# Kernel optimization log

Measured on AMD Instinct MI355X. Metric: run time of the kernel, lower is better.

The kernel has to match this reference:

```python
import jax, jax.numpy as jnp
import numpy as np

B, T, D, H, FC, A = 256, 128, 512, 1024, 1024, 32
LOG_STD_MIN, LOG_STD_MAX = -20.0, 2.0
EPS = 1e-5


def setup_inputs() -> dict:
    key = jax.random.key(0)
    ks = jax.random.split(key, 16)
    def w(k, shape, fan_in):
        return jax.random.normal(k, shape, jnp.float32) / np.float32(np.sqrt(fan_in))
    return {
        "observations": jax.random.normal(ks[0], (B, T, D), jnp.float32),
        "hidden_state": jax.random.normal(ks[1], (B, H), jnp.float32),
        "episode_starts": jax.random.randint(ks[2], (B, T), 0, 2, jnp.int32),
        "ln_gamma": jnp.ones((D,), jnp.float32),
        "ln_beta": jnp.zeros((D,), jnp.float32),
        "W_fc": w(ks[3], (FC, D), D), "b_fc": jnp.zeros((FC,), jnp.float32),
        "W_ih": w(ks[4], (3 * H, FC), FC), "b_ih": jnp.zeros((3 * H,), jnp.float32),
        "W_hh": w(ks[5], (3 * H, H), H), "b_hh": jnp.zeros((3 * H,), jnp.float32),
        "W_out": w(ks[6], (H, H), H), "b_out": jnp.zeros((H,), jnp.float32),
        "W_mean": w(ks[7], (A, H), H) * 0.01, "b_mean": jnp.zeros((A,), jnp.float32),
        "W_ls": w(ks[8], (A, H), H) * 0.01, "b_ls": jnp.zeros((A,), jnp.float32),
    }


def reference(observations, hidden_state, episode_starts, ln_gamma, ln_beta,
              W_fc, b_fc, W_ih, b_ih, W_hh, b_hh, W_out, b_out,
              W_mean, b_mean, W_ls, b_ls):
    # LayerNorm over last dim (eps=1e-5, like nn.LayerNorm)
    mu = jnp.mean(observations, axis=-1, keepdims=True)
    var = jnp.mean(jnp.square(observations - mu), axis=-1, keepdims=True)
    x = (observations - mu) * jax.lax.rsqrt(var + EPS) * ln_gamma + ln_beta
    # fc_in + ReLU, then precompute GRU input-gate projections for all steps
    x = jax.nn.relu(jnp.einsum('btd,fd->btf', x, W_fc) + b_fc)          # (B,T,FC)
    xg = jnp.einsum('btf,gf->btg', x, W_ih) + b_ih                      # (B,T,3H)
    xg_t = jnp.swapaxes(xg, 0, 1)                                       # (T,B,3H)
    starts_t = jnp.swapaxes(episode_starts, 0, 1).astype(jnp.float32)   # (T,B)

    def step(h, inp):
        xg_s, st = inp
        h = h * (1.0 - st)[:, None]
        gh = h @ W_hh.T + b_hh                                           # (B,3H)
        xr, xz, xn = xg_s[:, :H], xg_s[:, H:2 * H], xg_s[:, 2 * H:]
        hr, hz, hn = gh[:, :H], gh[:, H:2 * H], gh[:, 2 * H:]
        r = jax.nn.sigmoid(xr + hr)
        z = jax.nn.sigmoid(xz + hz)
        n = jnp.tanh(xn + r * hn)
        h_new = (1.0 - z) * n + z * h
        out = jax.nn.relu(h_new @ W_out.T + b_out)
        return h_new, out

    h_final, outs = jax.lax.scan(step, hidden_state, (xg_t, starts_t))
    feats = jnp.swapaxes(outs, 0, 1)                                     # (B,T,H)
    means = jnp.einsum('bth,ah->bta', feats, W_mean) + b_mean
    log_std = jnp.clip(jnp.einsum('bth,ah->bta', feats, W_ls) + b_ls,
                       LOG_STD_MIN, LOG_STD_MAX)
    return means, log_std, h_final
```

## Files before the change

kernel.cpp:

```cpp
#include <hip/hip_runtime.h>
#include <hip/hip_bf16.h>

#define B_ 256
#define T_ 128
#define D_ 512
#define H_ 1024
#define FC_ 1024
#define A_ 32
#define NWG_ 256

typedef short bf16x8 __attribute__((ext_vector_type(8)));
typedef float f32x4 __attribute__((ext_vector_type(4)));

__device__ __forceinline__ float bf2f(unsigned short u) {
  return __uint_as_float(((unsigned)u) << 16);
}
__device__ __forceinline__ unsigned short f2bf(float x) {
  unsigned u = __float_as_uint(x);
  u = u + 0x7fffu + ((u >> 16) & 1u);
  return (unsigned short)(u >> 16);
}
__device__ __forceinline__ void unpack8(uint4 v, float* f) {
  f[0] = bf2f(v.x & 0xffff); f[1] = bf2f(v.x >> 16);
  f[2] = bf2f(v.y & 0xffff); f[3] = bf2f(v.y >> 16);
  f[4] = bf2f(v.z & 0xffff); f[5] = bf2f(v.z >> 16);
  f[6] = bf2f(v.w & 0xffff); f[7] = bf2f(v.w >> 16);
}
__device__ __forceinline__ uint4 pack8(const float* f) {
  uint4 v;
  v.x = (unsigned)f2bf(f[0]) | ((unsigned)f2bf(f[1]) << 16);
  v.y = (unsigned)f2bf(f[2]) | ((unsigned)f2bf(f[3]) << 16);
  v.z = (unsigned)f2bf(f[4]) | ((unsigned)f2bf(f[5]) << 16);
  v.w = (unsigned)f2bf(f[6]) | ((unsigned)f2bf(f[7]) << 16);
  return v;
}

__global__ __launch_bounds__(256) void detect_kernel(
    const unsigned short* __restrict__ obs, int* __restrict__ flag)
{
  __shared__ int cnt;
  if (threadIdx.x == 0) cnt = 0;
  __syncthreads();
  int c = 0;
  for (int i = threadIdx.x; i < 8192; i += 256) {
    unsigned e = (obs[i] >> 7) & 0xffu;
    if (e >= 0x86u) c++;
  }
  atomicAdd(&cnt, c);
  __syncthreads();
  if (threadIdx.x == 0) *flag = (cnt >= 64) ? 1 : 0;
}

struct CanonArgs {
  const void* src[14];
  unsigned short* dst[14];
  int ofs[15];
};
__global__ __launch_bounds__(256) void canon_kernel(CanonArgs a,
                                                    const int* __restrict__ flag)
{
  const int fl = *flag;
  const int i0 = (blockIdx.x * 256 + threadIdx.x) * 8;
  int t = 0;
  while (t < 14 && i0 >= a.ofs[t + 1]) t++;
  if (t >= 14) return;
  const int local = i0 - a.ofs[t];
  unsigned short* d = a.dst[t] + local;
  if (fl) {
    const float* s = (const float*)a.src[t] + local;
    #pragma unroll
    for (int e = 0; e < 8; e++) d[e] = f2bf(s[e]);
  } else {
    const unsigned short* s = (const unsigned short*)a.src[t] + local;
    #pragma unroll
    for (int e = 0; e < 8; e++) d[e] = s[e];
  }
}

__global__ __launch_bounds__(256) void ln_kernel(
    const void* __restrict__ obs,
    const unsigned short* __restrict__ gamma_,
    const unsigned short* __restrict__ beta_,
    unsigned short* __restrict__ xn, int t0, int tcShift,
    const int* __restrict__ flag)
{
  const int fl = *flag;
  const int lane = threadIdx.x & 63;
  const int rloc = blockIdx.x * 4 + (threadIdx.x >> 6);
  const int b  = rloc >> tcShift;
  const int tl = rloc & ((1 << tcShift) - 1);
  const int grow = b * T_ + t0 + tl;
  float f[8];
  if (fl) {
    const float* of = (const float*)obs + (size_t)grow * D_ + lane * 8;
    const float4 v0 = *(const float4*)of;
    const float4 v1 = *(const float4*)(of + 4);
    f[0] = v0.x; f[1] = v0.y; f[2] = v0.z; f[3] = v0.w;
    f[4] = v1.x; f[5] = v1.y; f[6] = v1.z; f[7] = v1.w;
  } else {
    uint4 v = *(const uint4*)((const unsigned short*)obs + (size_t)grow * D_ + lane * 8);
    unpack8(v, f);
  }
  float s = 0.f, ss = 0.f;
  #pragma unroll
  for (int i = 0; i < 8; i++) { s += f[i]; ss += f[i] * f[i]; }
  #pragma unroll
  for (int off = 32; off > 0; off >>= 1) {
    s  += __shfl_xor(s,  off, 64);
    ss += __shfl_xor(ss, off, 64);
  }
  const float mu  = s * (1.0f / D_);
  const float var = ss * (1.0f / D_) - mu * mu;
  const float inv = rsqrtf(var + 1e-5f);
  float g[8], b8[8];
  unpack8(*(const uint4*)(gamma_ + lane * 8), g);
  unpack8(*(const uint4*)(beta_  + lane * 8), b8);
  float o[8];
  #pragma unroll
  for (int i = 0; i < 8; i++) o[i] = (f[i] - mu) * inv * g[i] + b8[i];
  *(uint4*)(xn + (size_t)rloc * D_ + lane * 8) = pack8(o);
}

__global__ __launch_bounds__(256) void gemm_tn(
    const unsigned short* __restrict__ A, const unsigned short* __restrict__ Bm,
    const unsigned short* __restrict__ bias, unsigned short* __restrict__ C,
    int M, int N, int K, int relu)
{
  __shared__ short As[128][40];
  __shared__ short Bs[128][40];
  const int tid  = threadIdx.x;
  const int wave = tid >> 6, lane = tid & 63;
  const int quad = lane >> 4, l15 = lane & 15;
  const int m0 = blockIdx.y * 128, n0 = blockIdx.x * 128;
  const int wm = (wave >> 1) * 64, wn = (wave & 1) * 64;
  const int lrow = tid >> 2, lk = (tid & 3) * 8;
  f32x4 acc[4][4] = {};
  const size_t a0 = (size_t)(m0 + lrow) * K + lk;
  const size_t a1 = (size_t)(m0 + lrow + 64) * K + lk;
  const size_t b0 = (size_t)(n0 + lrow) * K + lk;
  const size_t b1 = (size_t)(n0 + lrow + 64) * K + lk;
  for (int k0 = 0; k0 < K; k0 += 32) {
    __syncthreads();
    *(uint4*)&As[lrow][lk]      = *(const uint4*)(A  + a0 + k0);
    *(uint4*)&As[lrow + 64][lk] = *(const uint4*)(A  + a1 + k0);
    *(uint4*)&Bs[lrow][lk]      = *(const uint4*)(Bm + b0 + k0);
    *(uint4*)&Bs[lrow + 64][lk] = *(const uint4*)(Bm + b1 + k0);
    __syncthreads();
    bf16x8 af[4], bfv[4];
    #pragma unroll
    for (int i = 0; i < 4; i++) af[i]  = *(const bf16x8*)&As[wm + i * 16 + l15][quad * 8];
    #pragma unroll
    for (int j = 0; j < 4; j++) bfv[j] = *(const bf16x8*)&Bs[wn + j * 16 + l15][quad * 8];
    #pragma unroll
    for (int i = 0; i < 4; i++)
      #pragma unroll
      for (int j = 0; j < 4; j++)
        acc[i][j] = __builtin_amdgcn_mfma_f32_16x16x32_bf16(af[i], bfv[j], acc[i][j], 0, 0, 0);
  }
  #pragma unroll
  for (int j = 0; j < 4; j++) {
    const int col = n0 + wn + j * 16 + l15;
    const float bj = bias ? bf2f(bias[col]) : 0.0f;
    #pragma unroll
    for (int i = 0; i < 4; i++) {
      const int row = m0 + wm + i * 16 + quad * 4;
      #pragma unroll
      for (int r = 0; r < 4; r++) {
        float v = acc[i][j][r] + bj;
        if (relu) v = fmaxf(v, 0.0f);
        C[(size_t)(row + r) * N + col] = f2bf(v);
      }
    }
  }
}

__global__ __launch_bounds__(256, 1) void gru_scan(
    const unsigned short* __restrict__ xg,
    const int* __restrict__ starts,
    const unsigned short* __restrict__ Whh,
    const unsigned short* __restrict__ bhh,
    float* __restrict__ hf,
    unsigned long long* __restrict__ hb0,
    unsigned long long* __restrict__ hb1,
    unsigned short* __restrict__ hall,
    int t0, int Tc,
    int* __restrict__ flags)
{
  __shared__ short Ws[3 * 16 * 1032];
  __shared__ short Hs[64 * 136];
  __shared__ unsigned sbits[64][4];
  const int tid  = threadIdx.x;
  const int wg   = blockIdx.x;
  const int jb   = wg & 63, bb = wg >> 6;
  const int j0   = jb * 16, b0 = bb * 64;
  const int wave = tid >> 6, lane = tid & 63;
  const int quad = lane >> 4, l15 = lane & 15;

  for (int c = tid; c < 48 * 128; c += 256) {
    const int row = c >> 7;
    const int kc  = (c & 127) * 8;
    const int g = row >> 4, jj = row & 15;
    *(uint4*)&Ws[row * 1032 + kc] =
        *(const uint4*)(Whh + (size_t)(g * H_ + j0 + jj) * H_ + kc);
  }
  for (int c = tid; c < 64 * 4; c += 256) {
    const int row = c >> 2, w = c & 3;
    unsigned m = 0;
    #pragma unroll
    for (int bi = 0; bi < 32; bi++)
      m |= (starts[(b0 + row) * T_ + w * 32 + bi] ? 1u : 0u) << bi;
    sbits[row][w] = m;
  }
  const float br = bf2f(bhh[j0 + l15]);
  const float bz = bf2f(bhh[H_ + j0 + l15]);
  const float bn = bf2f(bhh[2 * H_ + j0 + l15]);
  const int col = j0 + l15;

  const int r0 = wave * 16 + quad * 4;
  float hreg[4];
  #pragma unroll
  for (int r = 0; r < 4; r++)
    hreg[r] = hf[(size_t)(b0 + r0 + r) * H_ + col];

  __syncthreads();

  for (int tl = 0; tl < Tc; tl++) {
    const int t = t0 + tl;
    const unsigned long long* hin = (t & 1) ? hb1 : hb0;
    unsigned* hout_u = (unsigned*)((t & 1) ? hb0 : hb1);

    float xr[4], xz[4], xnv[4];
    #pragma unroll
    for (int r = 0; r < 4; r++) {
      const size_t xrow = ((size_t)(b0 + r0 + r) * Tc + tl) * (3 * H_);
      xr[r]  = bf2f(xg[xrow + col]);
      xz[r]  = bf2f(xg[xrow + H_ + col]);
      xnv[r] = bf2f(xg[xrow + 2 * H_ + col]);
    }

    unsigned long long pf[8];
    #pragma unroll
    for (int u = 0; u < 8; u++) {
      const int c = tid + u * 256;
      const int row = c >> 5, kc = (c & 31) * 4;
      pf[u] = __hip_atomic_load(
          &hin[(((size_t)(b0 + row)) * H_ + kc) >> 2],
          __ATOMIC_RELAXED, __HIP_MEMORY_SCOPE_AGENT);
    }

    f32x4 acc[3] = {};
    const unsigned tw = (unsigned)(t >> 5), tb = (unsigned)(t & 31);
    for (int kc0 = 0; kc0 < H_; kc0 += 128) {
      __syncthreads();
      #pragma unroll
      for (int u = 0; u < 8; u++) {
        const int c = tid + u * 256;
        const int row = c >> 5, kc = (c & 31) * 4;
        unsigned long long v = pf[u];
        if ((sbits[row][tw] >> tb) & 1u) v = 0ull;
        *(unsigned long long*)&Hs[row * 136 + kc] = v;
      }
      __syncthreads();
      if (kc0 + 128 < H_) {
        #pragma unroll
        for (int u = 0; u < 8; u++) {
          const int c = tid + u * 256;
          const int row = c >> 5, kc = (c & 31) * 4;
          pf[u] = __hip_atomic_load(
              &hin[(((size_t)(b0 + row)) * H_ + kc0 + 128 + kc) >> 2],
              __ATOMIC_RELAXED, __HIP_MEMORY_SCOPE_AGENT);
        }
      }
      #pragma unroll
      for (int kk = 0; kk < 128; kk += 32) {
        bf16x8 a = *(const bf16x8*)&Hs[(wave * 16 + l15) * 136 + kk + quad * 8];
        #pragma unroll
        for (int g = 0; g < 3; g++) {
          bf16x8 b = *(const bf16x8*)&Ws[(g * 16 + l15) * 1032 + kc0 + kk + quad * 8];
          acc[g] = __builtin_amdgcn_mfma_f32_16x16x32_bf16(a, b, acc[g], 0, 0, 0);
        }
      }
    }

    #pragma unroll
    for (int r = 0; r < 4; r++) {
      const int lrow = r0 + r;
      const int b = b0 + lrow;
      const float kb = ((sbits[lrow][tw] >> tb) & 1u) ? 0.0f : 1.0f;
      const float hr = acc[0][r] + br;
      const float hz = acc[1][r] + bz;
      const float hn = acc[2][r] + bn;
      const float rg = 1.0f / (1.0f + __expf(-(xr[r] + hr)));
      const float zg = 1.0f / (1.0f + __expf(-(xz[r] + hz)));
      const float ng = tanhf(xnv[r] + rg * hn);
      const float hv = (1.0f - zg) * ng + zg * (hreg[r] * kb);
      hreg[r] = hv;
      const unsigned mine = (unsigned)f2bf(hv);
      const unsigned other = (unsigned)__shfl_xor((int)mine, 1, 64);
      if ((l15 & 1) == 0) {
        const unsigned packed = mine | (other << 16);
        __hip_atomic_store(&hout_u[((size_t)b * H_ + col) >> 1], packed,
                           __ATOMIC_RELAXED, __HIP_MEMORY_SCOPE_AGENT);
        ((unsigned*)hall)[(((size_t)b * Tc + tl) * H_ + col) >> 1] = packed;
      }
    }

    const int my = t0 + tl + 1;
    __builtin_amdgcn_s_waitcnt(0);
    __syncthreads();
    if (tid == 0)
      __hip_atomic_store(&flags[wg * 32], my, __ATOMIC_RELAXED,
                         __HIP_MEMORY_SCOPE_AGENT);
    if (tid < 64) {
      while (__hip_atomic_load(&flags[(bb * 64 + tid) * 32], __ATOMIC_RELAXED,
                               __HIP_MEMORY_SCOPE_AGENT) < my)
        __builtin_amdgcn_s_sleep(1);
    }
    __syncthreads();
  }

  #pragma unroll
  for (int r = 0; r < 4; r++)
    hf[(size_t)(b0 + r0 + r) * H_ + col] = hreg[r];
}

__global__ __launch_bounds__(256) void heads_kernel(
    const unsigned short* __restrict__ feats,
    const unsigned short* __restrict__ Wm, const unsigned short* __restrict__ bm,
    const unsigned short* __restrict__ Wl, const unsigned short* __restrict__ bl,
    void* __restrict__ outbuf, int t0, int tcShift, const int* __restrict__ flag)
{
  __shared__ short Fs[64][40];
  __shared__ short Ws[64][40];
  const int fl = *flag;
  const int tid  = threadIdx.x;
  const int wave = tid >> 6, lane = tid & 63;
  const int quad = lane >> 4, l15 = lane & 15;
  const int m0 = blockIdx.x * 64;
  const int lrow = tid >> 2, lk = (tid & 3) * 8;
  f32x4 acc[4] = {};
  for (int k0 = 0; k0 < H_; k0 += 32) {
    __syncthreads();
    *(uint4*)&Fs[lrow][lk] = *(const uint4*)(feats + (size_t)(m0 + lrow) * H_ + k0 + lk);
    const unsigned short* wsrc = (lrow < 32)
        ? (Wm + (size_t)lrow * H_ + k0 + lk)
        : (Wl + (size_t)(lrow - 32) * H_ + k0 + lk);
    *(uint4*)&Ws[lrow][lk] = *(const uint4*)wsrc;
    __syncthreads();
    bf16x8 af = *(const bf16x8*)&Fs[wave * 16 + l15][quad * 8];
    #pragma unroll
    for (int j = 0; j < 4; j++) {
      bf16x8 bfv = *(const bf16x8*)&Ws[j * 16 + l15][quad * 8];
      acc[j] = __builtin_amdgcn_mfma_f32_16x16x32_bf16(af, bfv, acc[j], 0, 0, 0);
    }
  }
  const int tcMask = (1 << tcShift) - 1;
  const size_t lstdBase = (size_t)B_ * T_ * A_;
  #pragma unroll
  for (int j = 0; j < 4; j++) {
    const int col = j * 16 + l15;
    #pragma unroll
    for (int r = 0; r < 4; r++) {
      const int row = m0 + wave * 16 + quad * 4 + r;
      const int grow = (row >> tcShift) * T_ + t0 + (row & tcMask);
      float v = acc[j][r];
      size_t idx;
      if (col < 32) {
        v += bf2f(bm[col]);
        idx = (size_t)grow * A_ + col;
      } else {
        v += bf2f(bl[col - 32]);
        v = fminf(fmaxf(v, -20.0f), 2.0f);
        idx = lstdBase + (size_t)grow * A_ + (col - 32);
      }
      if (fl) ((float*)outbuf)[idx] = v;
      else    ((unsigned short*)outbuf)[idx] = f2bf(v);
    }
  }
}

__global__ __launch_bounds__(256) void h0_cast(const void* __restrict__ h0,
                                               float* __restrict__ hf,
                                               unsigned short* __restrict__ hb0,
                                               const int* __restrict__ flag) {
  const int fl = *flag;
  int i = blockIdx.x * 256 + threadIdx.x;
  float v = fl ? ((const float*)h0)[i] : bf2f(((const unsigned short*)h0)[i]);
  hf[i] = v;
  hb0[i] = f2bf(v);
}
__global__ __launch_bounds__(256) void hfin_store(const float* __restrict__ h,
                                                  void* __restrict__ outbuf,
                                                  const int* __restrict__ flag) {
  const int fl = *flag;
  const size_t base = 2ull * B_ * T_ * A_;
  int i = blockIdx.x * 256 + threadIdx.x;
  if (fl) ((float*)outbuf)[base + i] = h[i];
  else    ((unsigned short*)outbuf)[base + i] = f2bf(h[i]);
}

extern "C" void kernel_launch(void* const* d_in, const int* in_sizes, int n_in,
                              void* d_out, int out_size, void* d_ws, size_t ws_size,
                              hipStream_t stream)
{
  const void* obs    = d_in[0];
  const void* h0in   = d_in[1];
  const int*  starts = (const int*)d_in[2];
  const void* fsrc[14] = { d_in[5], d_in[7], d_in[9], d_in[11], d_in[13], d_in[15],
                           d_in[3], d_in[4], d_in[6], d_in[8], d_in[10], d_in[12],
                           d_in[14], d_in[16] };
  const int fn[14] = { FC_ * D_, 3 * H_ * FC_, 3 * H_ * H_, H_ * H_, A_ * H_, A_ * H_,
                       D_, D_, FC_, 3 * H_, 3 * H_, H_, A_, A_ };

  char* ws = (char*)d_ws;
  int* flag = (int*)ws;
  size_t cur = 256;
  unsigned short* cdst[14];
  for (int i = 0; i < 14; i++) {
    cdst[i] = (unsigned short*)(ws + cur);
    cur += (size_t)fn[i] * 2;
    cur = (cur + 255) & ~255ull;
  }
  const size_t chunkBase = cur;
  const size_t fixedTail = 1048576ull  + 2ull * 524288ull
                         + 32768ull ;

  int Tc = 1;
  for (int c = 32; c >= 1; c >>= 1) {
    size_t need = chunkBase + (size_t)c * 2883584ull + fixedTail;
    if (need <= ws_size) { Tc = c; break; }
  }
  int tcShift = 0;
  while ((1 << tcShift) < Tc) tcShift++;

  unsigned short* xn   = (unsigned short*)(ws + chunkBase);
  unsigned short* xfc  = (unsigned short*)(ws + chunkBase + (size_t)Tc * 262144ull);
  unsigned short* xg   = (unsigned short*)(ws + chunkBase + (size_t)Tc * 786432ull);
  unsigned short* hall = (unsigned short*)(ws + chunkBase + (size_t)Tc * 2359296ull);
  size_t o = chunkBase + (size_t)Tc * 2883584ull;
  float* hf           = (float*)(ws + o);           o += 1048576ull;
  unsigned short* hb0 = (unsigned short*)(ws + o);  o += 524288ull;
  unsigned short* hb1 = (unsigned short*)(ws + o);  o += 524288ull;
  int* flags          = (int*)(ws + o);
  unsigned short* feats = xg;

  const unsigned short *Wfc = cdst[0], *Wih = cdst[1], *Whh = cdst[2], *Wout = cdst[3];
  const unsigned short *Wmean = cdst[4], *Wls = cdst[5];
  const unsigned short *gam = cdst[6], *bet = cdst[7], *bfc = cdst[8], *bih = cdst[9];
  const unsigned short *bhh = cdst[10], *bout = cdst[11], *bmean = cdst[12], *bls = cdst[13];

  detect_kernel<<<dim3(1), dim3(256), 0, stream>>>((const unsigned short*)obs, flag);
  CanonArgs ca;
  int total = 0;
  for (int i = 0; i < 14; i++) {
    ca.src[i] = fsrc[i];
    ca.dst[i] = cdst[i];
    ca.ofs[i] = total;
    total += fn[i];
  }
  ca.ofs[14] = total;
  canon_kernel<<<dim3((total / 8 + 255) / 256), dim3(256), 0, stream>>>(ca, flag);
  h0_cast<<<dim3(B_ * H_ / 256), dim3(256), 0, stream>>>(h0in, hf, hb0, flag);
  hipMemsetAsync(flags, 0, 32768, stream);

  const int Mc = B_ * Tc;
  for (int t0 = 0; t0 < T_; t0 += Tc) {
    ln_kernel<<<dim3(Mc / 4), dim3(256), 0, stream>>>(obs, gam, bet, xn, t0, tcShift, flag);
    gemm_tn<<<dim3(FC_ / 128, Mc / 128), dim3(256), 0, stream>>>(
        xn, Wfc, bfc, xfc, Mc, FC_, D_, 1);
    gemm_tn<<<dim3(3 * H_ / 128, Mc / 128), dim3(256), 0, stream>>>(
        xfc, Wih, bih, xg, Mc, 3 * H_, FC_, 0);

    gru_scan<<<dim3(NWG_), dim3(256), 0, stream>>>(
        xg, starts, Whh, bhh, hf,
        (unsigned long long*)hb0, (unsigned long long*)hb1,
        hall, t0, Tc, flags);

    gemm_tn<<<dim3(H_ / 128, Mc / 128), dim3(256), 0, stream>>>(
        hall, Wout, bout, feats, Mc, H_, H_, 1);
    heads_kernel<<<dim3(Mc / 64), dim3(256), 0, stream>>>(
        feats, Wmean, bmean, Wls, bls, d_out, t0, tcShift, flag);
  }

  hfin_store<<<dim3(B_ * H_ / 256), dim3(256), 0, stream>>>(hf, d_out, flag);
}
```

Before: 1.885 ms.

## Load GRU hidden state directly into registers; use global_load_lds in GEMM

The GRU scan no longer stages the hidden state through shared memory with per-chunk barriers. Each wave now loads its own 16 rows of h straight into registers in MFMA operand layout, applies the episode-start mask with a bitwise AND, and runs all 32 k-steps without any syncthreads. Separately, the tiled GEMM uses direct global-to-LDS loads with an unpadded LDS layout, dropping the register round trip. The trade-offs are much higher register pressure in the scan (64 u64 values per lane) and possible LDS bank conflicts now that the GEMM tile rows are no longer padded.

```diff
diff --git a/kernel.cpp b/kernel.cpp
--- a/kernel.cpp
+++ b/kernel.cpp
@@ -11,6 +11,8 @@
 
 typedef short bf16x8 __attribute__((ext_vector_type(8)));
 typedef float f32x4 __attribute__((ext_vector_type(4)));
+typedef unsigned long long ull;
+typedef ull ullx2 __attribute__((ext_vector_type(2)));
 
 __device__ __forceinline__ float bf2f(unsigned short u) {
   return __uint_as_float(((unsigned)u) << 16);
@@ -126,31 +128,42 @@
     const unsigned short* __restrict__ bias, unsigned short* __restrict__ C,
     int M, int N, int K, int relu)
 {
-  __shared__ short As[128][40];
-  __shared__ short Bs[128][40];
+  __shared__ short As[128 * 32];
+  __shared__ short Bs[128 * 32];
   const int tid  = threadIdx.x;
   const int wave = tid >> 6, lane = tid & 63;
   const int quad = lane >> 4, l15 = lane & 15;
   const int m0 = blockIdx.y * 128, n0 = blockIdx.x * 128;
   const int wm = (wave >> 1) * 64, wn = (wave & 1) * 64;
-  const int lrow = tid >> 2, lk = (tid & 3) * 8;
+  const int srow = tid >> 2;
+  const int skc  = (tid & 3) * 8;
+  const size_t aoff0 = (size_t)(m0 + srow) * K + skc;
+  const size_t aoff1 = (size_t)(m0 + 64 + srow) * K + skc;
+  const size_t boff0 = (size_t)(n0 + srow) * K + skc;
+  const size_t boff1 = (size_t)(n0 + 64 + srow) * K + skc;
+  const int lb0 = wave * 512;
+  const int lb1 = 2048 + wave * 512;
   f32x4 acc[4][4] = {};
-  const size_t a0 = (size_t)(m0 + lrow) * K + lk;
-  const size_t a1 = (size_t)(m0 + lrow + 64) * K + lk;
-  const size_t b0 = (size_t)(n0 + lrow) * K + lk;
-  const size_t b1 = (size_t)(n0 + lrow + 64) * K + lk;
   for (int k0 = 0; k0 < K; k0 += 32) {
     __syncthreads();
-    *(uint4*)&As[lrow][lk]      = *(const uint4*)(A  + a0 + k0);
-    *(uint4*)&As[lrow + 64][lk] = *(const uint4*)(A  + a1 + k0);
-    *(uint4*)&Bs[lrow][lk]      = *(const uint4*)(Bm + b0 + k0);
-    *(uint4*)&Bs[lrow + 64][lk] = *(const uint4*)(Bm + b1 + k0);
+    __builtin_amdgcn_global_load_lds(
+        (const __attribute__((address_space(1))) unsigned*)(A + aoff0 + k0),
+        (__attribute__((address_space(3))) unsigned*)&As[lb0], 16, 0, 0);
+    __builtin_amdgcn_global_load_lds(
+        (const __attribute__((address_space(1))) unsigned*)(A + aoff1 + k0),
+        (__attribute__((address_space(3))) unsigned*)&As[lb1], 16, 0, 0);
+    __builtin_amdgcn_global_load_lds(
+        (const __attribute__((address_space(1))) unsigned*)(Bm + boff0 + k0),
+        (__attribute__((address_space(3))) unsigned*)&Bs[lb0], 16, 0, 0);
+    __builtin_amdgcn_global_load_lds(
+        (const __attribute__((address_space(1))) unsigned*)(Bm + boff1 + k0),
+        (__attribute__((address_space(3))) unsigned*)&Bs[lb1], 16, 0, 0);
     __syncthreads();
     bf16x8 af[4], bfv[4];
     #pragma unroll
-    for (int i = 0; i < 4; i++) af[i]  = *(const bf16x8*)&As[wm + i * 16 + l15][quad * 8];
-    #pragma unroll
-    for (int j = 0; j < 4; j++) bfv[j] = *(const bf16x8*)&Bs[wn + j * 16 + l15][quad * 8];
+    for (int i = 0; i < 4; i++) af[i]  = *(const bf16x8*)&As[(wm + i * 16 + l15) * 32 + quad * 8];
+    #pragma unroll
+    for (int j = 0; j < 4; j++) bfv[j] = *(const bf16x8*)&Bs[(wn + j * 16 + l15) * 32 + quad * 8];
     #pragma unroll
     for (int i = 0; i < 4; i++)
       #pragma unroll
@@ -180,14 +193,13 @@
     const unsigned short* __restrict__ Whh,
     const unsigned short* __restrict__ bhh,
     float* __restrict__ hf,
-    unsigned long long* __restrict__ hb0,
-    unsigned long long* __restrict__ hb1,
+    ull* __restrict__ hb0,
+    ull* __restrict__ hb1,
     unsigned short* __restrict__ hall,
     int t0, int Tc,
     int* __restrict__ flags)
 {
   __shared__ short Ws[3 * 16 * 1032];
-  __shared__ short Hs[64 * 136];
   __shared__ unsigned sbits[64][4];
   const int tid  = threadIdx.x;
   const int wg   = blockIdx.x;
@@ -222,12 +234,29 @@
   for (int r = 0; r < 4; r++)
     hreg[r] = hf[(size_t)(b0 + r0 + r) * H_ + col];
 
+  const int arow = wave * 16 + l15;
+  const size_t hrowbase = ((size_t)(b0 + arow)) << 8;
+  const short* wsb = &Ws[l15 * 1032 + quad * 8];
+
   __syncthreads();
 
   for (int tl = 0; tl < Tc; tl++) {
     const int t = t0 + tl;
-    const unsigned long long* hin = (t & 1) ? hb1 : hb0;
+    const ull* hin = (t & 1) ? hb1 : hb0;
     unsigned* hout_u = (unsigned*)((t & 1) ? hb0 : hb1);
+    const unsigned tw = (unsigned)(t >> 5), tb = (unsigned)(t & 31);
+
+    ull hu0[32], hu1[32];
+    {
+      const ull* hp = hin + hrowbase + quad * 2;
+      #pragma unroll
+      for (int j = 0; j < 32; j++) {
+        hu0[j] = __hip_atomic_load(hp + j * 8,     __ATOMIC_RELAXED,
+                                   __HIP_MEMORY_SCOPE_AGENT);
+        hu1[j] = __hip_atomic_load(hp + j * 8 + 1, __ATOMIC_RELAXED,
+                                   __HIP_MEMORY_SCOPE_AGENT);
+      }
+    }
 
     float xr[4], xz[4], xnv[4];
     #pragma unroll
@@ -238,48 +267,21 @@
       xnv[r] = bf2f(xg[xrow + 2 * H_ + col]);
     }
 
-    unsigned long long pf[8];
-    #pragma unroll
-    for (int u = 0; u < 8; u++) {
-      const int c = tid + u * 256;
-      const int row = c >> 5, kc = (c & 31) * 4;
-      pf[u] = __hip_atomic_load(
-          &hin[(((size_t)(b0 + row)) * H_ + kc) >> 2],
-          __ATOMIC_RELAXED, __HIP_MEMORY_SCOPE_AGENT);
-    }
+    const ull keep = ((sbits[arow][tw] >> tb) & 1u) ? 0ull : ~0ull;
 
     f32x4 acc[3] = {};
-    const unsigned tw = (unsigned)(t >> 5), tb = (unsigned)(t & 31);
-    for (int kc0 = 0; kc0 < H_; kc0 += 128) {
-      __syncthreads();
-      #pragma unroll
-      for (int u = 0; u < 8; u++) {
-        const int c = tid + u * 256;
-        const int row = c >> 5, kc = (c & 31) * 4;
-        unsigned long long v = pf[u];
-        if ((sbits[row][tw] >> tb) & 1u) v = 0ull;
-        *(unsigned long long*)&Hs[row * 136 + kc] = v;
-      }
-      __syncthreads();
-      if (kc0 + 128 < H_) {
-        #pragma unroll
-        for (int u = 0; u < 8; u++) {
-          const int c = tid + u * 256;
-          const int row = c >> 5, kc = (c & 31) * 4;
-          pf[u] = __hip_atomic_load(
-              &hin[(((size_t)(b0 + row)) * H_ + kc0 + 128 + kc) >> 2],
-              __ATOMIC_RELAXED, __HIP_MEMORY_SCOPE_AGENT);
-        }
-      }
-      #pragma unroll
-      for (int kk = 0; kk < 128; kk += 32) {
-        bf16x8 a = *(const bf16x8*)&Hs[(wave * 16 + l15) * 136 + kk + quad * 8];
-        #pragma unroll
-        for (int g = 0; g < 3; g++) {
-          bf16x8 b = *(const bf16x8*)&Ws[(g * 16 + l15) * 1032 + kc0 + kk + quad * 8];
-          acc[g] = __builtin_amdgcn_mfma_f32_16x16x32_bf16(a, b, acc[g], 0, 0, 0);
-        }
-      }
+    #pragma unroll
+    for (int j = 0; j < 32; j++) {
+      ullx2 u2;
+      u2.x = hu0[j] & keep;
+      u2.y = hu1[j] & keep;
+      const bf16x8 a = __builtin_bit_cast(bf16x8, u2);
+      acc[0] = __builtin_amdgcn_mfma_f32_16x16x32_bf16(
+          a, *(const bf16x8*)(wsb + 0 * 16512 + j * 32), acc[0], 0, 0, 0);
+      acc[1] = __builtin_amdgcn_mfma_f32_16x16x32_bf16(
+          a, *(const bf16x8*)(wsb + 1 * 16512 + j * 32), acc[1], 0, 0, 0);
+      acc[2] = __builtin_amdgcn_mfma_f32_16x16x32_bf16(
+          a, *(const bf16x8*)(wsb + 2 * 16512 + j * 32), acc[2], 0, 0, 0);
     }
 
     #pragma unroll
@@ -473,7 +475,7 @@
 
     gru_scan<<<dim3(NWG_), dim3(256), 0, stream>>>(
         xg, starts, Whh, bhh, hf,
-        (unsigned long long*)hb0, (unsigned long long*)hb1,
+        (ull*)hb0, (ull*)hb1,
         hall, t0, Tc, flags);
 
     gemm_tn<<<dim3(H_ / 128, Mc / 128), dim3(256), 0, stream>>>(
```

Result: slower. 2.274 ms (+20.6%).
